# Optimization experiments

Measured on AMD Instinct MI355X. Metric: run time of the kernel, lower is better.

## Reference

```python
import jax, jax.numpy as jnp
import numpy as np

B, T, C, H = 4, 4096, 1024, 128

def setup_inputs() -> dict:
    key = jax.random.key(0)
    kx, kk, kq, kv = jax.random.split(key, 4)
    scale = 1.0 / np.sqrt(C)  # mimic Linear init scale
    return {
        'x':  jax.random.normal(kx, (B, T, C), dtype=jnp.float32),
        'Wk': jax.random.normal(kk, (C, H), dtype=jnp.float32) * scale,
        'Wq': jax.random.normal(kq, (C, H), dtype=jnp.float32) * scale,
        'Wv': jax.random.normal(kv, (C, H), dtype=jnp.float32) * scale,
    }

def reference(x, Wk, Wq, Wv):
    # x: [B,T,C]; projections to [B,T,H]
    k = jnp.einsum('btc,ch->bth', x, Wk)
    q = jnp.einsum('btc,ch->bth', x, Wq)
    v = jnp.einsum('btc,ch->bth', x, Wv)
    scale = jnp.asarray(x.shape[-1] and (k.shape[-1] ** -0.5), dtype=x.dtype)
    # scores: [B,T,T]
    scores = jnp.einsum('bqh,bkh->bqk', q, k) * scale
    Tn = x.shape[1]
    causal = jnp.tril(jnp.ones((Tn, Tn), dtype=bool))
    scores = jnp.where(causal[None, :, :], scores, -jnp.inf)
    attn = jax.nn.softmax(scores, axis=-1)
    # dropout=0.0 -> identity
    out = jnp.einsum('bqk,bkh->bqh', attn, v)
    return out
```

## Files before the change

kernel.cpp:

```cpp
#include <hip/hip_runtime.h>
#include <hip/hip_bf16.h>
#include <math.h>

#define B_ 4
#define T_ 4096
#define C_ 1024
#define H_ 128
#define SCALE 0.08838834764831845f
#define SCL2  0.12752934464f

typedef __attribute__((ext_vector_type(8))) short bf16x8;
typedef __attribute__((ext_vector_type(4))) float f32x4;

__device__ __forceinline__ unsigned short f2bf(float f) {
    union { float f; unsigned u; } x; x.f = f;
    unsigned r = x.u + 0x7FFF + ((x.u >> 16) & 1);
    return (unsigned short)(r >> 16);
}
__device__ __forceinline__ float bf2f(unsigned short u) {
    union { unsigned u; float f; } x; x.u = ((unsigned)u) << 16;
    return x.f;
}
__device__ __forceinline__ unsigned cvt_pk_bf16(float a, float b) {
    unsigned r;
    asm("v_cvt_pk_bf16_f32 %0, %1, %2" : "=v"(r) : "v"(a), "v"(b));
    return r;
}
__device__ __forceinline__ void cvt16(const float4& a, const float4& b,
                                      const float4& c, const float4& d,
                                      unsigned* t) {
    t[0]=cvt_pk_bf16(a.x,a.y); t[1]=cvt_pk_bf16(a.z,a.w);
    t[2]=cvt_pk_bf16(b.x,b.y); t[3]=cvt_pk_bf16(b.z,b.w);
    t[4]=cvt_pk_bf16(c.x,c.y); t[5]=cvt_pk_bf16(c.z,c.w);
    t[6]=cvt_pk_bf16(d.x,d.y); t[7]=cvt_pk_bf16(d.z,d.w);
}

#define GLOAD16(gsrc, ldst)                                                        \
    __builtin_amdgcn_global_load_lds(                                              \
        (const __attribute__((address_space(1))) unsigned int*)(gsrc),             \
        (__attribute__((address_space(3))) unsigned int*)(ldst), 16, 0, 0)

__global__ __launch_bounds__(256) void wtrans_kernel(
        const float* __restrict__ Wk, const float* __restrict__ Wq,
        const float* __restrict__ Wv, unsigned short* __restrict__ Wt) {
    int tid = blockIdx.x * 256 + threadIdx.x;
    int t = tid >> 17;
    int r = tid & 131071;
    int c = r >> 7;
    int h = r & 127;
    const float* W = (t == 0) ? Wk : (t == 1) ? Wq : Wv;
    Wt[t * 131072 + h * 1024 + c] = f2bf(W[r]);
}

__global__ __launch_bounds__(256, 2) void qkv_gemm3(
        const float* __restrict__ x, const unsigned short* __restrict__ Wt,
        unsigned short* __restrict__ qkv, unsigned short* __restrict__ vT) {
    __shared__ unsigned short As[2][64][72];
    __shared__ unsigned short Bs[2][192][64];

    const int nsw = blockIdx.x;
    const int sw = (nsw & 7) * 64 + (nsw >> 3);
    const int m0 = (sw >> 1) * 64;
    const int nh = sw & 1;

    const int tid = threadIdx.x;
    const int lane = tid & 63;
    const int w = tid >> 6;
    const int fr = lane & 15;
    const int fq = lane >> 4;

    const int xrow = tid >> 2, xco = (tid & 3) * 16;
    const float* xsrc = x + (long)(m0 + xrow) * C_ + xco;
    const int brl = lane >> 3;
    const int bcolb = (((lane & 7) ^ brl) << 4);
    unsigned short* const bs_flat = &Bs[0][0][0];
    const unsigned short* wbase = Wt + (long)(nh * 192) * 1024;

    f32x4 acc[3][4];
#pragma unroll
    for (int i = 0; i < 3; i++)
#pragma unroll
        for (int rf = 0; rf < 4; rf++) acc[i][rf] = f32x4{0.f, 0.f, 0.f, 0.f};

    float4 xa0, xa1, xa2, xa3, xb0, xb1, xb2, xb3;
    xa0 = ((const float4*)xsrc)[0]; xa1 = ((const float4*)xsrc)[1];
    xa2 = ((const float4*)xsrc)[2]; xa3 = ((const float4*)xsrc)[3];
#pragma unroll
    for (int i = 0; i < 6; i++)
        GLOAD16(wbase + (long)(48*w + 8*i + brl) * 1024 + (bcolb >> 1),
                bs_flat + (w*6 + i) * 512);
    {
        unsigned tw[8];
        cvt16(xa0, xa1, xa2, xa3, tw);
        *(uint4*)&As[0][xrow][xco]     = uint4{tw[0], tw[1], tw[2], tw[3]};
        *(uint4*)&As[0][xrow][xco + 8] = uint4{tw[4], tw[5], tw[6], tw[7]};
    }
    {
        const float* xs = xsrc + 64;
        xa0 = ((const float4*)xs)[0]; xa1 = ((const float4*)xs)[1];
        xa2 = ((const float4*)xs)[2]; xa3 = ((const float4*)xs)[3];
    }

    int cur = 0;
    for (int k = 0; k < 16; ++k) {
        __syncthreads();
        const bool more  = (k + 1) < 16;
        const bool more2 = (k + 2) < 16;
        if (more) {
            if (more2) {
                const float* xs = xsrc + (k + 2) * 64;
                xb0 = ((const float4*)xs)[0]; xb1 = ((const float4*)xs)[1];
                xb2 = ((const float4*)xs)[2]; xb3 = ((const float4*)xs)[3];
            }
            const int boff = (cur ^ 1) * 12288;
#pragma unroll
            for (int i = 0; i < 6; i++)
                GLOAD16(wbase + (long)(48*w + 8*i + brl) * 1024 + (k + 1) * 64 + (bcolb >> 1),
                        bs_flat + boff + (w*6 + i) * 512);
            if (more2) asm volatile("s_waitcnt vmcnt(10)" ::: "memory");
            else       asm volatile("s_waitcnt vmcnt(6)" ::: "memory");
        } else {
            asm volatile("s_waitcnt vmcnt(0)" ::: "memory");
        }
        __syncthreads();

        const char* bsb = (const char*)bs_flat + cur * 24576;
        __builtin_amdgcn_s_setprio(1);
#pragma unroll
        for (int kk = 0; kk < 2; kk++) {
            bf16x8 a[4], bb[3];
#pragma unroll
            for (int rf = 0; rf < 4; rf++)
                a[rf] = *(const bf16x8*)&As[cur][rf*16 + fr][kk*32 + fq*8];
#pragma unroll
            for (int i = 0; i < 3; i++) {
                int row = (w*3 + i) * 16 + fr;
                bb[i] = *(const bf16x8*)(bsb + row*128 + ((((kk<<2) + fq) ^ (fr & 7)) << 4));
            }
#pragma unroll
            for (int i = 0; i < 3; i++)
#pragma unroll
                for (int rf = 0; rf < 4; rf++)
                    acc[i][rf] = __builtin_amdgcn_mfma_f32_16x16x32_bf16(
                        a[rf], bb[i], acc[i][rf], 0, 0, 0);
        }
        __builtin_amdgcn_s_setprio(0);

        if (more) {
            unsigned tw[8];
            cvt16(xa0, xa1, xa2, xa3, tw);
            *(uint4*)&As[cur ^ 1][xrow][xco]     = uint4{tw[0], tw[1], tw[2], tw[3]};
            *(uint4*)&As[cur ^ 1][xrow][xco + 8] = uint4{tw[4], tw[5], tw[6], tw[7]};
            xa0 = xb0; xa1 = xb1; xa2 = xb2; xa3 = xb3;
        }
        cur ^= 1;
    }

#pragma unroll
    for (int i = 0; i < 3; i++) {
        int nfg = nh*12 + w*3 + i;
        int t = nfg >> 3;
        int col = (nfg & 7) * 16 + fr;
        if (t < 2) {
#pragma unroll
            for (int rf = 0; rf < 4; rf++)
#pragma unroll
                for (int r = 0; r < 4; r++) {
                    int row = m0 + rf*16 + fq*4 + r;
                    qkv[(long)t * 2097152 + (long)row * 128 + col] = f2bf(acc[i][rf][r]);
                }
        } else {
            const int bb_ = m0 >> 12;
            const int trow = m0 & 4095;
#pragma unroll
            for (int rf = 0; rf < 4; rf++) {
                uint2 uu;
                uu.x = cvt_pk_bf16(acc[i][rf][0], acc[i][rf][1]);
                uu.y = cvt_pk_bf16(acc[i][rf][2], acc[i][rf][3]);
                *(uint2*)(vT + ((long)(bb_*128 + col)) * 4096 + trow + rf*16 + fq*4) = uu;
            }
        }
    }
}

__global__ __launch_bounds__(512, 4) void flash9_kernel(
        const unsigned short* __restrict__ qkv,
        const unsigned short* __restrict__ vT,
        unsigned short* __restrict__ po0, unsigned short* __restrict__ po1,
        unsigned short* __restrict__ po2, unsigned short* __restrict__ po3,
        float* __restrict__ pm, float* __restrict__ pl) {
    __shared__ unsigned short k_lds[2][64][128];
    __shared__ unsigned short v_lds[2][128][64];

    const int n = blockIdx.x;
    const int half = n >> 8;
    const int m = n & 255;
    const int b = (m & 7) >> 1;
    const int r = ((m >> 3) << 1) | (m & 1);
    const int jj = r & 31;
    const int pq = r >> 5;
    const int qt = half ? (31 - jj) : jj;
    const int p = half * 2 + pq;
    const int q0 = qt * 128;
    const int ntt = (qt + 1) * 2;
    const int t0 = (p * ntt) >> 2;
    const int t1 = ((p + 1) * ntt) >> 2;

    const int tid = threadIdx.x;
    const int w = tid >> 6;
    const int lane = tid & 63;
    const int fr = lane & 15;
    const int fq = lane >> 4;

    const unsigned short* kbase = qkv + (long)b * T_ * H_;
    const unsigned short* vbase = vT + (long)b * H_ * T_;

    const int kcolb0 = ((lane & 15) << 4) ^ ((((lane >> 4)) & 7) << 4);
    const int kcolb1 = ((lane & 15) << 4) ^ (((4 + (lane >> 4)) & 7) << 4);
    const int krl = lane >> 4;
    const int vrl = lane >> 3;
    const int vcolb = ((lane & 7) << 4) ^ (vrl << 4);
    unsigned short* const klds_flat = &k_lds[0][0][0];
    unsigned short* const vlds_flat = &v_lds[0][0][0];
    const int scol = ((fq ^ (fr & 7)) << 4);

    bf16x8 qf[4];
    {
        const unsigned short* qptr = qkv + 2097152 + ((long)b*T_ + q0 + w*16 + fr) * H_;
#pragma unroll
        for (int ks = 0; ks < 4; ks++)
            qf[ks] = *(const bf16x8*)(qptr + ks*32 + fq*8);
    }

    bf16x8 ones;
    {
        union { unsigned short s[8]; bf16x8 v; } oc;
#pragma unroll
        for (int i = 0; i < 8; i++) oc.s[i] = 0x3F80;
        ones = oc.v;
    }

    f32x4 acc[8];
#pragma unroll
    for (int i = 0; i < 8; i++) acc[i] = f32x4{0.f, 0.f, 0.f, 0.f};
    f32x4 acc_l = f32x4{0.f, 0.f, 0.f, 0.f};
    float m_r = -INFINITY;
    const int qrow = q0 + w*16 + fr;

    int cur = 0;
    if (t0 < t1) {
        const int kv0 = t0 * 64;
#pragma unroll
        for (int i = 0; i < 2; i++) {
            int kcolb = i ? kcolb1 : kcolb0;
            GLOAD16(kbase + (long)(kv0 + 8*w + 4*i + krl) * 128 + (kcolb >> 1),
                    klds_flat + w*1024 + i*512);
            GLOAD16(vbase + (long)(16*w + 8*i + vrl) * 4096 + kv0 + (vcolb >> 1),
                    vlds_flat + w*1024 + i*512);
        }
    }

    for (int t = t0; t < t1; ++t) {
        const int kv0 = t * 64;
        asm volatile("s_waitcnt vmcnt(0)" ::: "memory");
        __syncthreads();
        if (t + 1 < t1) {
            const int kv0n = kv0 + 64;
            const int boff = (cur ^ 1) * 8192;
#pragma unroll
            for (int i = 0; i < 2; i++) {
                int kcolb = i ? kcolb1 : kcolb0;
                GLOAD16(kbase + (long)(kv0n + 8*w + 4*i + krl) * 128 + (kcolb >> 1),
                        klds_flat + boff + w*1024 + i*512);
                GLOAD16(vbase + (long)(16*w + 8*i + vrl) * 4096 + kv0n + (vcolb >> 1),
                        vlds_flat + boff + w*1024 + i*512);
            }
        }

        const char* kl = (const char*)k_lds + cur*16384 + fr*256;
        const char* vl = (const char*)v_lds + cur*16384 + fr*128;

        f32x4 s[4];
#pragma unroll
        for (int sf = 0; sf < 4; sf++) s[sf] = f32x4{0.f,0.f,0.f,0.f};
        __builtin_amdgcn_s_setprio(1);
#pragma unroll
        for (int sf = 0; sf < 4; sf++)
#pragma unroll
            for (int ks = 0; ks < 4; ks++) {
                bf16x8 kf = *(const bf16x8*)(kl + sf*4096 + (scol ^ (ks << 6)));
                s[sf] = __builtin_amdgcn_mfma_f32_16x16x32_bf16(kf, qf[ks], s[sf], 0, 0, 0);
            }
        __builtin_amdgcn_s_setprio(0);

        float pmax = -INFINITY;
        if (kv0 + 63 > q0 + 16*w) {
#pragma unroll
            for (int sf = 0; sf < 4; sf++)
#pragma unroll
                for (int rr = 0; rr < 4; rr++) {
                    int kv = kv0 + sf*16 + fq*4 + rr;
                    float sv = s[sf][rr] * SCL2;
                    sv = (kv > qrow) ? -INFINITY : sv;
                    s[sf][rr] = sv;
                    pmax = fmaxf(pmax, sv);
                }
        } else {
#pragma unroll
            for (int sf = 0; sf < 4; sf++)
#pragma unroll
                for (int rr = 0; rr < 4; rr++) {
                    float sv = s[sf][rr] * SCL2;
                    s[sf][rr] = sv;
                    pmax = fmaxf(pmax, sv);
                }
        }

        const bool skip = __all((m_r > -1e37f) & (pmax - m_r <= 11.5f));
        float msub;
        if (skip) {
            msub = m_r;
        } else {
            float mx = fmaxf(pmax, __shfl_xor(pmax, 16, 64));
            mx = fmaxf(mx, __shfl_xor(mx, 32, 64));
            float mn = fmaxf(m_r, mx);
            msub = (mn == -INFINITY) ? 0.f : mn;
            float alpha = exp2f(m_r - msub);
            m_r = mn;
#pragma unroll
            for (int hf = 0; hf < 8; hf++)
#pragma unroll
                for (int rr = 0; rr < 4; rr++) acc[hf][rr] *= alpha;
#pragma unroll
            for (int rr = 0; rr < 4; rr++) acc_l[rr] *= alpha;
        }

        float pv[4][4];
#pragma unroll
        for (int sf = 0; sf < 4; sf++)
#pragma unroll
            for (int rr = 0; rr < 4; rr++)
                pv[sf][rr] = exp2f(s[sf][rr] - msub);

        unsigned pw[8];
#pragma unroll
        for (int sf = 0; sf < 4; sf++) {
            pw[2*sf]   = cvt_pk_bf16(pv[sf][0], pv[sf][1]);
            pw[2*sf+1] = cvt_pk_bf16(pv[sf][2], pv[sf][3]);
        }
        unsigned pbu[2][4];
        pbu[0][0]=0;pbu[0][1]=0;pbu[0][2]=0;pbu[0][3]=0;
        pbu[1][0]=0;pbu[1][1]=0;pbu[1][2]=0;pbu[1][3]=0;
        const int L1 = fr + 16 * ((fq & 1) * 2);
        const int L2 = L1 + 16;
        const int sel = (fq >> 1) & 1;
#pragma unroll
        for (int sf = 0; sf < 4; sf++) {
            unsigned w0 = (unsigned)__shfl((int)pw[2*sf],   L1, 64);
            unsigned w1 = (unsigned)__shfl((int)pw[2*sf+1], L1, 64);
            unsigned w2 = (unsigned)__shfl((int)pw[2*sf],   L2, 64);
            unsigned w3 = (unsigned)__shfl((int)pw[2*sf+1], L2, 64);
            if ((sf & 1) == sel) {
                int k2 = sf >> 1;
                pbu[k2][0] = w0; pbu[k2][1] = w1; pbu[k2][2] = w2; pbu[k2][3] = w3;
            }
        }
        union { unsigned u[4]; bf16x8 v; } pb0c, pb1c;
#pragma unroll
        for (int i = 0; i < 4; i++) { pb0c.u[i] = pbu[0][i]; pb1c.u[i] = pbu[1][i]; }
        bf16x8 pb0 = pb0c.v, pb1 = pb1c.v;

        __builtin_amdgcn_s_setprio(1);
#pragma unroll
        for (int hf = 0; hf < 8; hf++) {
            bf16x8 vf0 = *(const bf16x8*)(vl + hf*2048 + scol);
            bf16x8 vf1 = *(const bf16x8*)(vl + hf*2048 + (scol ^ 64));
            acc[hf] = __builtin_amdgcn_mfma_f32_16x16x32_bf16(vf0, pb0, acc[hf], 0, 0, 0);
            acc[hf] = __builtin_amdgcn_mfma_f32_16x16x32_bf16(vf1, pb1, acc[hf], 0, 0, 0);
        }
        acc_l = __builtin_amdgcn_mfma_f32_16x16x32_bf16(ones, pb0, acc_l, 0, 0, 0);
        acc_l = __builtin_amdgcn_mfma_f32_16x16x32_bf16(ones, pb1, acc_l, 0, 0, 0);
        __builtin_amdgcn_s_setprio(0);
        cur ^= 1;
    }

    unsigned short* po = (p == 0) ? po0 : (p == 1) ? po1 : (p == 2) ? po2 : po3;
    const float l_r = acc_l[0];
    float linv = (l_r > 0.f) ? (1.0f / l_r) : 0.f;
    const long obase = ((long)b * T_ + qrow) * H_;
#pragma unroll
    for (int hf = 0; hf < 8; hf++) {
        uint2 uu;
        uu.x = cvt_pk_bf16(acc[hf][0] * linv, acc[hf][1] * linv);
        uu.y = cvt_pk_bf16(acc[hf][2] * linv, acc[hf][3] * linv);
        *(uint2*)(po + obase + hf*16 + fq*4) = uu;
    }
    if (fq == 0) {
        pm[p * 16384 + b * T_ + qrow] = m_r;
        pl[p * 16384 + b * T_ + qrow] = l_r;
    }
}

__global__ __launch_bounds__(256) void combine4_kernel(
        const unsigned short* __restrict__ po0,
        const unsigned short* __restrict__ po1,
        const unsigned short* __restrict__ po2,
        const unsigned short* __restrict__ po3,
        const float* __restrict__ pm, const float* __restrict__ pl,
        float* __restrict__ out) {
    int idx = blockIdx.x * 256 + threadIdx.x;
    int row = idx >> 4;
    int seg = idx & 15;
    float mv[4], lv[4];
#pragma unroll
    for (int i = 0; i < 4; i++) { mv[i] = pm[i*16384 + row]; lv[i] = pl[i*16384 + row]; }
    float m = fmaxf(fmaxf(mv[0], mv[1]), fmaxf(mv[2], mv[3]));
    float wv[4]; float tot = 0.f;
#pragma unroll
    for (int i = 0; i < 4; i++) {
        wv[i] = (lv[i] > 0.f) ? exp2f(mv[i] - m) * lv[i] : 0.f;
        tot += wv[i];
    }
    float inv = 1.0f / tot;
    long off = (long)row * H_ + seg * 8;
    unsigned short ua[8], ub[8], uc[8], ud[8];
    *(uint4*)ua = *(const uint4*)(po0 + off);
    *(uint4*)ub = *(const uint4*)(po1 + off);
    *(uint4*)uc = *(const uint4*)(po2 + off);
    *(uint4*)ud = *(const uint4*)(po3 + off);
    float* o = out + off;
#pragma unroll
    for (int j2 = 0; j2 < 8; j2++)
        o[j2] = inv * (wv[0] * bf2f(ua[j2]) + wv[1] * bf2f(ub[j2]) +
                       wv[2] * bf2f(uc[j2]) + wv[3] * bf2f(ud[j2]));
}

extern "C" void kernel_launch(void* const* d_in, const int* in_sizes, int n_in,
                              void* d_out, int out_size, void* d_ws, size_t ws_size,
                              hipStream_t stream) {
    (void)in_sizes; (void)n_in; (void)out_size; (void)ws_size;
    const float* x  = (const float*)d_in[0];
    const float* Wk = (const float*)d_in[1];
    const float* Wq = (const float*)d_in[2];
    const float* Wv = (const float*)d_in[3];
    float* out = (float*)d_out;

    unsigned short* Wt  = (unsigned short*)d_ws;
    unsigned short* qkv = Wt + 393216;
    unsigned short* vT  = qkv + 6291456;
    unsigned short* po0 = vT + 2097152;
    unsigned short* po1 = po0 + 2097152;
    unsigned short* po3 = po1 + 2097152;
    unsigned short* po2 = qkv + 4194304;
    float* pm = (float*)d_ws;
    float* pl = pm + 65536;

    wtrans_kernel<<<1536, 256, 0, stream>>>(Wk, Wq, Wv, Wt);
    qkv_gemm3<<<512, 256, 0, stream>>>(x, Wt, qkv, vT);
    flash9_kernel<<<512, 512, 0, stream>>>(qkv, vT, po0, po1, po2, po3, pm, pl);
    combine4_kernel<<<1024, 256, 0, stream>>>(po0, po1, po2, po3, pm, pl, out);
}
```

Measured before the change: 80.24 us.

## Merge QKV GEMM column halves into 512-thread blocks and use raw v_exp_f32

```diff
diff --git a/kernel.cpp b/kernel.cpp
--- a/kernel.cpp
+++ b/kernel.cpp
@@ -26,13 +26,14 @@
     asm("v_cvt_pk_bf16_f32 %0, %1, %2" : "=v"(r) : "v"(a), "v"(b));
     return r;
 }
-__device__ __forceinline__ void cvt16(const float4& a, const float4& b,
-                                      const float4& c, const float4& d,
-                                      unsigned* t) {
+__device__ __forceinline__ float vexp2(float x) {
+    float r;
+    asm("v_exp_f32 %0, %1" : "=v"(r) : "v"(x));
+    return r;
+}
+__device__ __forceinline__ void cvt8(const float4& a, const float4& b, unsigned* t) {
     t[0]=cvt_pk_bf16(a.x,a.y); t[1]=cvt_pk_bf16(a.z,a.w);
     t[2]=cvt_pk_bf16(b.x,b.y); t[3]=cvt_pk_bf16(b.z,b.w);
-    t[4]=cvt_pk_bf16(c.x,c.y); t[5]=cvt_pk_bf16(c.z,c.w);
-    t[6]=cvt_pk_bf16(d.x,d.y); t[7]=cvt_pk_bf16(d.z,d.w);
 }
 
 #define GLOAD16(gsrc, ldst)                                                        \
@@ -52,16 +53,14 @@
     Wt[t * 131072 + h * 1024 + c] = f2bf(W[r]);
 }
 
-__global__ __launch_bounds__(256, 2) void qkv_gemm3(
+__global__ __launch_bounds__(512, 2) void qkv_gemm5(
         const float* __restrict__ x, const unsigned short* __restrict__ Wt,
         unsigned short* __restrict__ qkv, unsigned short* __restrict__ vT) {
     __shared__ unsigned short As[2][64][72];
-    __shared__ unsigned short Bs[2][192][64];
+    __shared__ unsigned short Bs[2][384][64];
 
     const int nsw = blockIdx.x;
-    const int sw = (nsw & 7) * 64 + (nsw >> 3);
-    const int m0 = (sw >> 1) * 64;
-    const int nh = sw & 1;
+    const int m0 = ((nsw & 7) * 32 + (nsw >> 3)) * 64;
 
     const int tid = threadIdx.x;
     const int lane = tid & 63;
@@ -69,12 +68,11 @@
     const int fr = lane & 15;
     const int fq = lane >> 4;
 
-    const int xrow = tid >> 2, xco = (tid & 3) * 16;
+    const int xrow = tid >> 3, xco = (tid & 7) * 8;
     const float* xsrc = x + (long)(m0 + xrow) * C_ + xco;
     const int brl = lane >> 3;
     const int bcolb = (((lane & 7) ^ brl) << 4);
     unsigned short* const bs_flat = &Bs[0][0][0];
-    const unsigned short* wbase = Wt + (long)(nh * 192) * 1024;
 
     f32x4 acc[3][4];
 #pragma unroll
@@ -82,23 +80,20 @@
 #pragma unroll
         for (int rf = 0; rf < 4; rf++) acc[i][rf] = f32x4{0.f, 0.f, 0.f, 0.f};
 
-    float4 xa0, xa1, xa2, xa3, xb0, xb1, xb2, xb3;
+    float4 xa0, xa1, xb0, xb1;
     xa0 = ((const float4*)xsrc)[0]; xa1 = ((const float4*)xsrc)[1];
-    xa2 = ((const float4*)xsrc)[2]; xa3 = ((const float4*)xsrc)[3];
 #pragma unroll
     for (int i = 0; i < 6; i++)
-        GLOAD16(wbase + (long)(48*w + 8*i + brl) * 1024 + (bcolb >> 1),
+        GLOAD16(Wt + (long)(48*w + 8*i + brl) * 1024 + (bcolb >> 1),
                 bs_flat + (w*6 + i) * 512);
     {
-        unsigned tw[8];
-        cvt16(xa0, xa1, xa2, xa3, tw);
-        *(uint4*)&As[0][xrow][xco]     = uint4{tw[0], tw[1], tw[2], tw[3]};
-        *(uint4*)&As[0][xrow][xco + 8] = uint4{tw[4], tw[5], tw[6], tw[7]};
+        unsigned tw[4];
+        cvt8(xa0, xa1, tw);
+        *(uint4*)&As[0][xrow][xco] = uint4{tw[0], tw[1], tw[2], tw[3]};
     }
     {
         const float* xs = xsrc + 64;
         xa0 = ((const float4*)xs)[0]; xa1 = ((const float4*)xs)[1];
-        xa2 = ((const float4*)xs)[2]; xa3 = ((const float4*)xs)[3];
     }
 
     int cur = 0;
@@ -110,21 +105,20 @@
             if (more2) {
                 const float* xs = xsrc + (k + 2) * 64;
                 xb0 = ((const float4*)xs)[0]; xb1 = ((const float4*)xs)[1];
-                xb2 = ((const float4*)xs)[2]; xb3 = ((const float4*)xs)[3];
-            }
-            const int boff = (cur ^ 1) * 12288;
+            }
+            const int boff = (cur ^ 1) * 24576;
 #pragma unroll
             for (int i = 0; i < 6; i++)
-                GLOAD16(wbase + (long)(48*w + 8*i + brl) * 1024 + (k + 1) * 64 + (bcolb >> 1),
+                GLOAD16(Wt + (long)(48*w + 8*i + brl) * 1024 + (k + 1) * 64 + (bcolb >> 1),
                         bs_flat + boff + (w*6 + i) * 512);
-            if (more2) asm volatile("s_waitcnt vmcnt(10)" ::: "memory");
+            if (more2) asm volatile("s_waitcnt vmcnt(8)" ::: "memory");
             else       asm volatile("s_waitcnt vmcnt(6)" ::: "memory");
         } else {
             asm volatile("s_waitcnt vmcnt(0)" ::: "memory");
         }
         __syncthreads();
 
-        const char* bsb = (const char*)bs_flat + cur * 24576;
+        const char* bsb = (const char*)bs_flat + cur * 49152;
         __builtin_amdgcn_s_setprio(1);
 #pragma unroll
         for (int kk = 0; kk < 2; kk++) {
@@ -147,18 +141,17 @@
         __builtin_amdgcn_s_setprio(0);
 
         if (more) {
-            unsigned tw[8];
-            cvt16(xa0, xa1, xa2, xa3, tw);
-            *(uint4*)&As[cur ^ 1][xrow][xco]     = uint4{tw[0], tw[1], tw[2], tw[3]};
-            *(uint4*)&As[cur ^ 1][xrow][xco + 8] = uint4{tw[4], tw[5], tw[6], tw[7]};
-            xa0 = xb0; xa1 = xb1; xa2 = xb2; xa3 = xb3;
+            unsigned tw[4];
+            cvt8(xa0, xa1, tw);
+            *(uint4*)&As[cur ^ 1][xrow][xco] = uint4{tw[0], tw[1], tw[2], tw[3]};
+            xa0 = xb0; xa1 = xb1;
         }
         cur ^= 1;
     }
 
 #pragma unroll
     for (int i = 0; i < 3; i++) {
-        int nfg = nh*12 + w*3 + i;
+        int nfg = w*3 + i;
         int t = nfg >> 3;
         int col = (nfg & 7) * 16 + fr;
         if (t < 2) {
@@ -325,7 +318,7 @@
             mx = fmaxf(mx, __shfl_xor(mx, 32, 64));
             float mn = fmaxf(m_r, mx);
             msub = (mn == -INFINITY) ? 0.f : mn;
-            float alpha = exp2f(m_r - msub);
+            float alpha = vexp2(m_r - msub);
             m_r = mn;
 #pragma unroll
             for (int hf = 0; hf < 8; hf++)
@@ -340,7 +333,7 @@
         for (int sf = 0; sf < 4; sf++)
 #pragma unroll
             for (int rr = 0; rr < 4; rr++)
-                pv[sf][rr] = exp2f(s[sf][rr] - msub);
+                pv[sf][rr] = vexp2(s[sf][rr] - msub);
 
         unsigned pw[8];
 #pragma unroll
@@ -456,7 +449,7 @@
     float* pl = pm + 65536;
 
     wtrans_kernel<<<1536, 256, 0, stream>>>(Wk, Wq, Wv, Wt);
-    qkv_gemm3<<<512, 256, 0, stream>>>(x, Wt, qkv, vT);
+    qkv_gemm5<<<256, 512, 0, stream>>>(x, Wt, qkv, vT);
     flash9_kernel<<<512, 512, 0, stream>>>(qkv, vT, po0, po1, po2, po3, pm, pl);
     combine4_kernel<<<1024, 256, 0, stream>>>(po0, po1, po2, po3, pm, pl, out);
 }
```

New measurement: 85.11 us. +6.1%, slower.
